# Kernel tuning notes

Measured on AMD Instinct MI355X. Metric: run time of the kernel, lower is better.

Reference implementation:

```python
import jax, jax.numpy as jnp
import numpy as np

N_EMBD = 384
NUM_HEADS = 6
HEAD_SIZE = 64


def setup_inputs() -> dict:
    key = jax.random.key(0)
    k1, k2, k3, k4 = jax.random.split(key, 4)
    B, T = 32, 1024
    x = jax.random.normal(k1, (B, T, N_EMBD), dtype=jnp.float32)
    # torch Linear(n_embd, 3*n_embd, bias=False): store as [in, out]
    s_attn = 1.0 / np.sqrt(N_EMBD)
    W_attn = jax.random.uniform(k2, (N_EMBD, 3 * N_EMBD), dtype=jnp.float32, minval=-s_attn, maxval=s_attn)
    W_proj = jax.random.uniform(k3, (N_EMBD, N_EMBD), dtype=jnp.float32, minval=-s_attn, maxval=s_attn)
    b_proj = jax.random.uniform(k4, (N_EMBD,), dtype=jnp.float32, minval=-s_attn, maxval=s_attn)
    return {"x": x, "W_attn": W_attn, "W_proj": W_proj, "b_proj": b_proj}


def reference(x, W_attn, W_proj, b_proj):
    B, T, C = x.shape
    H, D = NUM_HEADS, HEAD_SIZE
    qkv = x @ W_attn                      # [B, T, 3C]
    q, k, v = jnp.split(qkv, 3, axis=2)   # each [B, T, C]
    # [B, H, T, D]
    q = q.reshape(B, T, H, D).transpose(0, 2, 1, 3)
    k = k.reshape(B, T, H, D).transpose(0, 2, 1, 3)
    v = v.reshape(B, T, H, D).transpose(0, 2, 1, 3)
    scale = 1.0 / jnp.sqrt(jnp.asarray(D, dtype=x.dtype))
    scores = jnp.einsum("bhqd,bhkd->bhqk", q, k) * scale  # [B, H, T, T]
    causal = jnp.tril(jnp.ones((T, T), dtype=bool))
    scores = jnp.where(causal, scores, jnp.asarray(-jnp.inf, dtype=scores.dtype))
    attn = jax.nn.softmax(scores, axis=-1)
    y = jnp.einsum("bhqk,bhkd->bhqd", attn, v)             # [B, H, T, D]
    y = y.transpose(0, 2, 1, 3).reshape(B, T, C)
    # dropout is inactive in eval mode
    return y @ W_proj + b_proj
```

## Files before the change

### kernel.cpp

```cpp
#include <hip/hip_runtime.h>
#include <hip/hip_bf16.h>

#define DEV __device__ __forceinline__

typedef __attribute__((ext_vector_type(4))) float f32x4;
typedef __bf16 bf16x8 __attribute__((ext_vector_type(8)));

static DEV unsigned short f2bf(float f) {
    union { float f; unsigned u; } x; x.f = f;
    unsigned r = x.u + 0x7fffu + ((x.u >> 16) & 1u);
    return (unsigned short)(r >> 16);
}

static DEV f32x4 zero4() { f32x4 v; v[0] = 0.f; v[1] = 0.f; v[2] = 0.f; v[3] = 0.f; return v; }

#define GL1(p) ((const __attribute__((address_space(1))) void*)(p))
#define LDS3(p) ((__attribute__((address_space(3))) void*)(p))


__global__ __launch_bounds__(256) void k_prep(
    const float* __restrict__ x, unsigned short* __restrict__ xb,
    const float* __restrict__ Wa, unsigned short* __restrict__ WaT,
    const float* __restrict__ Wp, unsigned short* __restrict__ WpT)
{
    int i = blockIdx.x * 256 + threadIdx.x;
    if (i < 3145728) {
        float4 v = reinterpret_cast<const float4*>(x)[i];
        ushort4 o;
        o.x = f2bf(v.x); o.y = f2bf(v.y); o.z = f2bf(v.z); o.w = f2bf(v.w);
        reinterpret_cast<ushort4*>(xb)[i] = o;
    } else if (i < 3145728 + 442368) {
        int j = i - 3145728;
        int n = j / 384, k = j - n * 384;
        WaT[j] = f2bf(Wa[(size_t)k * 1152 + n]);
    } else if (i < 3145728 + 442368 + 147456) {
        int j = i - (3145728 + 442368);
        int n = j / 384, k = j - n * 384;
        WpT[j] = f2bf(Wp[(size_t)k * 384 + n]);
    }
}


template <int SWAP>
static DEV void gemm_mainloop(
    const unsigned short* __restrict__ A,
    const unsigned short* __restrict__ B,
    int m0, int n0, int tid,
    f32x4 (&acc)[4][4],
    unsigned short (&lA)[128][64], unsigned short (&lB)[128][64])
{
    const int K = 384;
    const int w = tid >> 6, lane = tid & 63;
    const int wm = (w >> 1) * 64, wn = (w & 1) * 64;
    const int lr = lane & 15, lg = lane >> 4;
    const int lrow = lane >> 3;
    const int lcol = ((lane & 7) ^ lrow) * 8;

    for (int kb = 0; kb < K; kb += 64) {
        __syncthreads();
#pragma unroll
        for (int c = 0; c < 4; ++c) {
            int rb = (w * 4 + c) * 8;
            __builtin_amdgcn_global_load_lds(GL1(&A[(size_t)(m0 + rb + lrow) * K + kb + lcol]),
                                             LDS3(&lA[rb][0]), 16, 0, 0);
            __builtin_amdgcn_global_load_lds(GL1(&B[(size_t)(n0 + rb + lrow) * K + kb + lcol]),
                                             LDS3(&lB[rb][0]), 16, 0, 0);
        }
        __syncthreads();

        bf16x8 af[4][2], bfr[4][2];
#pragma unroll
        for (int kc = 0; kc < 2; ++kc) {
#pragma unroll
            for (int t = 0; t < 4; ++t) {
                int ga = ((kc * 4 + lg) ^ (lr & 7)) * 8;
                af[t][kc]  = *(const bf16x8*)&lA[wm + t * 16 + lr][ga];
                bfr[t][kc] = *(const bf16x8*)&lB[wn + t * 16 + lr][ga];
            }
        }
#pragma unroll
        for (int kc = 0; kc < 2; ++kc)
#pragma unroll
            for (int mt = 0; mt < 4; ++mt)
#pragma unroll
                for (int nt = 0; nt < 4; ++nt)
                    acc[mt][nt] = SWAP
                        ? __builtin_amdgcn_mfma_f32_16x16x32_bf16(bfr[nt][kc], af[mt][kc], acc[mt][nt], 0, 0, 0)
                        : __builtin_amdgcn_mfma_f32_16x16x32_bf16(af[mt][kc], bfr[nt][kc], acc[mt][nt], 0, 0, 0);
    }
}


__global__ __launch_bounds__(256) void k_gemm_qkv(
    const unsigned short* __restrict__ A,
    const unsigned short* __restrict__ B,
    unsigned short* __restrict__ Qb, unsigned short* __restrict__ Kb,
    unsigned short* __restrict__ Vb)
{
    __shared__ unsigned short lA[128][64];
    __shared__ unsigned short lB[128][64];

    const int tid = threadIdx.x;
    const int m0 = blockIdx.x * 128, n0 = blockIdx.y * 128;
    const int w = tid >> 6, lane = tid & 63;
    const int wm = (w >> 1) * 64, wn = (w & 1) * 64;
    const int lr = lane & 15, lg = lane >> 4;

    f32x4 acc[4][4];
#pragma unroll
    for (int i = 0; i < 4; i++)
#pragma unroll
        for (int j = 0; j < 4; j++) acc[i][j] = zero4();

    if (blockIdx.y < 6) {
        gemm_mainloop<1>(A, B, m0, n0, tid, acc, lA, lB);
        const int which = blockIdx.y / 3;
#pragma unroll
        for (int mt = 0; mt < 4; ++mt) {
            int row = m0 + wm + mt * 16 + lr;
            int bb = row >> 10, tloc = row & 1023;
#pragma unroll
            for (int nt = 0; nt < 4; ++nt) {
                int col = n0 + wn + nt * 16 + lg * 4;
                int c = col - which * 384;
                int hh = c >> 6, d0 = c & 63;
                size_t bh = (size_t)bb * 6 + hh;
                int kc = (d0 >> 5) & 1;
                int ln = (tloc & 15) + 16 * ((d0 >> 3) & 3);
                int e0 = d0 & 7;
                union { __bf16 h4[4]; uint2 u; } pk;
                if (which == 0) {
#pragma unroll
                    for (int r = 0; r < 4; ++r)
                        pk.h4[r] = (__bf16)(acc[mt][nt][r] * 0.18033688f);
                    int qt = tloc >> 5, fmt = (tloc >> 4) & 1;
                    *(uint2*)&Qb[((((bh * 32 + qt) * 2 + fmt) * 2 + kc) * 64 + ln) * 8 + e0] = pk.u;
                } else {
#pragma unroll
                    for (int r = 0; r < 4; ++r)
                        pk.h4[r] = (__bf16)acc[mt][nt][r];
                    int ktt = tloc >> 6, fnt = (tloc >> 4) & 3;
                    *(uint2*)&Kb[((((bh * 16 + ktt) * 4 + fnt) * 2 + kc) * 64 + ln) * 8 + e0] = pk.u;
                }
            }
        }
    } else {
        gemm_mainloop<0>(A, B, m0, n0, tid, acc, lA, lB);
#pragma unroll
        for (int nt = 0; nt < 4; ++nt) {
            int col = n0 + wn + nt * 16 + lr;
            int c = col - 768;
            int hh = c >> 6, d = c & 63;
            int fnt = d >> 4;
#pragma unroll
            for (int mt = 0; mt < 4; ++mt) {
                int row0 = m0 + wm + mt * 16 + lg * 4;
                int bb = row0 >> 10, t0 = row0 & 1023;
                size_t bh = (size_t)bb * 6 + hh;
                int ktt = t0 >> 6, kc = (t0 >> 5) & 1, e0 = t0 & 7;
                int ln = (d & 15) + 16 * ((t0 >> 3) & 3);
                union { __bf16 h4[4]; uint2 u; } pk;
#pragma unroll
                for (int r = 0; r < 4; ++r)
                    pk.h4[r] = (__bf16)acc[mt][nt][r];
                *(uint2*)&Vb[((((bh * 16 + ktt) * 4 + fnt) * 2 + kc) * 64 + ln) * 8 + e0] = pk.u;
            }
        }
    }
}


__global__ __launch_bounds__(256) void k_gemm_proj(
    const unsigned short* __restrict__ A,
    const unsigned short* __restrict__ B,
    const float* __restrict__ bias, float* __restrict__ Out)
{
    __shared__ unsigned short lA[128][64];
    __shared__ unsigned short lB[128][64];

    const int tid = threadIdx.x;
    const int m0 = blockIdx.x * 128, n0 = blockIdx.y * 128;
    const int w = tid >> 6, lane = tid & 63;
    const int wm = (w >> 1) * 64, wn = (w & 1) * 64;
    const int lr = lane & 15, lg = lane >> 4;

    f32x4 acc[4][4];
#pragma unroll
    for (int i = 0; i < 4; i++)
#pragma unroll
        for (int j = 0; j < 4; j++) acc[i][j] = zero4();

    gemm_mainloop<1>(A, B, m0, n0, tid, acc, lA, lB);

#pragma unroll
    for (int mt = 0; mt < 4; ++mt) {
        int row = m0 + wm + mt * 16 + lr;
#pragma unroll
        for (int nt = 0; nt < 4; ++nt) {
            int col = n0 + wn + nt * 16 + lg * 4;
            f32x4 bv = *(const f32x4*)&bias[col];
            f32x4 ov;
#pragma unroll
            for (int r = 0; r < 4; ++r) ov[r] = acc[mt][nt][r] + bv[r];
            *(f32x4*)&Out[(size_t)row * 384 + col] = ov;
        }
    }
}


template <int NTM, bool MASK>
static DEV void attn_tile(
    const unsigned short* lKt, const unsigned short* lVt, unsigned short* lPw,
    const bf16x8 (&qf)[2][2], f32x4 (&o)[2][4], float (&ls)[2],
    int kt, int qw, int lane)
{
    constexpr int KCM = NTM / 2;
    const int lr = lane & 15, lg = lane >> 4;

    bf16x8 kf[NTM][2];
#pragma unroll
    for (int nt = 0; nt < NTM; ++nt)
#pragma unroll
        for (int kc = 0; kc < 2; ++kc)
            kf[nt][kc] = *(const bf16x8*)&lKt[(nt * 2 + kc) * 512 + lane * 8];

    bf16x8 vf[4][KCM];
#pragma unroll
    for (int nt = 0; nt < 4; ++nt)
#pragma unroll
        for (int kc = 0; kc < KCM; ++kc)
            vf[nt][kc] = *(const bf16x8*)&lVt[(nt * 2 + kc) * 512 + lane * 8];

    f32x4 st[2][NTM];
#pragma unroll
    for (int mt = 0; mt < 2; ++mt)
#pragma unroll
        for (int nt = 0; nt < NTM; ++nt) st[mt][nt] = zero4();

#pragma unroll
    for (int kc = 0; kc < 2; ++kc)
#pragma unroll
        for (int mt = 0; mt < 2; ++mt)
#pragma unroll
            for (int nt = 0; nt < NTM; ++nt)
                st[mt][nt] = __builtin_amdgcn_mfma_f32_16x16x32_bf16(kf[nt][kc], qf[mt][kc], st[mt][nt], 0, 0, 0);

#pragma unroll
    for (int mt = 0; mt < 2; ++mt) {
#pragma unroll
        for (int nt = 0; nt < NTM; ++nt) {
            union { __bf16 hh[4]; uint2 u; } pk;
            float e[4];
#pragma unroll
            for (int r = 0; r < 4; ++r) {
                float ev = __builtin_amdgcn_exp2f(st[mt][nt][r]);
                if (MASK) {
                    int kg = kt * 64 + nt * 16 + lg * 4 + r;
                    int qg = qw + mt * 16 + lr;
                    if (kg > qg) ev = 0.f;
                }
                e[r] = ev;
                pk.hh[r] = (__bf16)ev;
            }
            ls[mt] += (e[0] + e[1]) + (e[2] + e[3]);
            int ln2 = lr + 16 * ((nt & 1) * 2 + (lg >> 1));
            *(uint2*)&lPw[(mt * 2 + (nt >> 1)) * 512 + ln2 * 8 + (lg & 1) * 4] = pk.u;
        }
    }

    bf16x8 pf[2][KCM];
#pragma unroll
    for (int mt = 0; mt < 2; ++mt)
#pragma unroll
        for (int kc = 0; kc < KCM; ++kc)
            pf[mt][kc] = *(const bf16x8*)&lPw[(mt * 2 + kc) * 512 + lane * 8];

#pragma unroll
    for (int mt = 0; mt < 2; ++mt)
#pragma unroll
        for (int nt = 0; nt < 4; ++nt)
#pragma unroll
            for (int kc = 0; kc < KCM; ++kc)
                o[mt][nt] = __builtin_amdgcn_mfma_f32_16x16x32_bf16(pf[mt][kc], vf[nt][kc], o[mt][nt], 0, 0, 0);
}

__global__ __launch_bounds__(256, 3) void k_attn(
    const unsigned short* __restrict__ Qf,
    const unsigned short* __restrict__ Kf,
    const unsigned short* __restrict__ Vf,
    unsigned short* __restrict__ Y)
{
    __shared__ unsigned short lK[2][4096];
    __shared__ unsigned short lV[2][4096];
    __shared__ unsigned short lPf[4][2048];

    const int tid = threadIdx.x;
    const int w = tid >> 6, lane = tid & 63;
    const int lr = lane & 15, lg = lane >> 4;
    const int bh = blockIdx.x;
    const int g = 7 - blockIdx.y;
    const int qt = 4 * g + w;
    const int qw = qt * 32;
    const int nkt = qt / 2 + 1;
    const int nsteps = 2 * g + 2;
    const int b = bh / 6, h = bh - b * 6;

    const unsigned short* Kbh = Kf + (size_t)bh * 65536;
    const unsigned short* Vbh = Vf + (size_t)bh * 65536;

    bf16x8 qf[2][2];
#pragma unroll
    for (int mt = 0; mt < 2; ++mt)
#pragma unroll
        for (int kc = 0; kc < 2; ++kc)
            qf[mt][kc] = *(const bf16x8*)&Qf[((((size_t)bh * 32 + qt) * 2 + mt) * 2 + kc) * 512 + lane * 8];

    f32x4 o[2][4];
    float ls[2] = {0.f, 0.f};
#pragma unroll
    for (int mt = 0; mt < 2; ++mt)
#pragma unroll
        for (int nt = 0; nt < 4; ++nt) o[mt][nt] = zero4();

#pragma unroll
    for (int i = 0; i < 2; ++i) {
        __builtin_amdgcn_global_load_lds(GL1(Kbh + (size_t)w * 1024 + i * 512 + lane * 8),
                                         LDS3(&lK[0][w * 1024 + i * 512]), 16, 0, 0);
        __builtin_amdgcn_global_load_lds(GL1(Vbh + (size_t)w * 1024 + i * 512 + lane * 8),
                                         LDS3(&lV[0][w * 1024 + i * 512]), 16, 0, 0);
    }

    for (int kt = 0; kt < nsteps; ++kt) {
        __syncthreads();
        if (kt + 1 < nsteps) {
            int nb = (kt + 1) & 1;
#pragma unroll
            for (int i = 0; i < 2; ++i) {
                __builtin_amdgcn_global_load_lds(GL1(Kbh + (size_t)(kt + 1) * 4096 + w * 1024 + i * 512 + lane * 8),
                                                 LDS3(&lK[nb][w * 1024 + i * 512]), 16, 0, 0);
                __builtin_amdgcn_global_load_lds(GL1(Vbh + (size_t)(kt + 1) * 4096 + w * 1024 + i * 512 + lane * 8),
                                                 LDS3(&lV[nb][w * 1024 + i * 512]), 16, 0, 0);
            }
        }
        if (kt < nkt) {
            const unsigned short* lKt = lK[kt & 1];
            const unsigned short* lVt = lV[kt & 1];
            if (kt == nkt - 1) {
                if (qt & 1) attn_tile<4, true>(lKt, lVt, lPf[w], qf, o, ls, kt, qw, lane);
                else        attn_tile<2, true>(lKt, lVt, lPf[w], qf, o, ls, kt, qw, lane);
            } else {
                attn_tile<4, false>(lKt, lVt, lPf[w], qf, o, ls, kt, qw, lane);
            }
        }
    }

    float inv[2];
#pragma unroll
    for (int mt = 0; mt < 2; ++mt) {
        float s = ls[mt];
        s += __shfl_xor(s, 16);
        s += __shfl_xor(s, 32);
        inv[mt] = 1.0f / s;
    }
#pragma unroll
    for (int mt = 0; mt < 2; ++mt) {
        float iv[4];
#pragma unroll
        for (int r = 0; r < 4; ++r) iv[r] = __shfl(inv[mt], lg * 4 + r);
#pragma unroll
        for (int nt = 0; nt < 4; ++nt)
#pragma unroll
            for (int r = 0; r < 4; ++r) {
                int qrow = qw + mt * 16 + lg * 4 + r;
                int col = h * 64 + nt * 16 + lr;
                Y[((size_t)b * 1024 + qrow) * 384 + col] = f2bf(o[mt][nt][r] * iv[r]);
            }
    }
}


extern "C" void kernel_launch(void* const* d_in, const int* in_sizes, int n_in,
                              void* d_out, int out_size, void* d_ws, size_t ws_size,
                              hipStream_t stream)
{
    const float* x  = (const float*)d_in[0];
    const float* Wa = (const float*)d_in[1];
    const float* Wp = (const float*)d_in[2];
    const float* bp = (const float*)d_in[3];
    float* out = (float*)d_out;

    char* ws = (char*)d_ws;
    unsigned short* xb  = (unsigned short*)(ws);
    unsigned short* WaT = (unsigned short*)(ws + 25165824);
    unsigned short* WpT = (unsigned short*)(ws + 26050560);
    unsigned short* Qb  = (unsigned short*)(ws + 26345472);
    unsigned short* Kb  = (unsigned short*)(ws + 51511296);
    unsigned short* Vtb = (unsigned short*)(ws + 76677120);

    k_prep<<<14592, 256, 0, stream>>>(x, xb, Wa, WaT, Wp, WpT);
    k_gemm_qkv<<<dim3(256, 9), 256, 0, stream>>>(xb, WaT, Qb, Kb, Vtb);
    k_attn<<<dim3(192, 8), 256, 0, stream>>>(Qb, Kb, Vtb, xb);
    k_gemm_proj<<<dim3(256, 3), 256, 0, stream>>>(xb, WpT, bp, out);
}
```

Before: 125.1 us.

## Double-buffer GEMM LDS loads, raise MFMA priority, and transpose attention output accumulation

The GEMM mainloop gets double-buffered LDS tiles, so the next K slice is loaded while the current one is computed, and one barrier per iteration is removed. The attention PV MFMA swaps its operands, so the output accumulator is laid out with the query row on lr. That lets the epilogue write four contiguous bf16 values per store and drops the per-element shuffles. s_setprio is raised around the MFMA blocks to favour issuing matrix instructions. Doubling the GEMM LDS use may lower occupancy, and the single barrier per iteration relies on the async LDS loads finishing before the next sync.

```diff
diff --git a/kernel.cpp b/kernel.cpp
--- a/kernel.cpp
+++ b/kernel.cpp
@@ -47,7 +47,7 @@
     const unsigned short* __restrict__ B,
     int m0, int n0, int tid,
     f32x4 (&acc)[4][4],
-    unsigned short (&lA)[128][64], unsigned short (&lB)[128][64])
+    unsigned short (&lA)[2][128][64], unsigned short (&lB)[2][128][64])
 {
     const int K = 384;
     const int w = tid >> 6, lane = tid & 63;
@@ -56,17 +56,24 @@
     const int lrow = lane >> 3;
     const int lcol = ((lane & 7) ^ lrow) * 8;
 
-    for (int kb = 0; kb < K; kb += 64) {
+#define STAGE_GEMM(buf, kb)                                                                       \
+    {                                                                                             \
+        _Pragma("unroll") for (int c = 0; c < 4; ++c) {                                           \
+            int rb = (w * 4 + c) * 8;                                                             \
+            __builtin_amdgcn_global_load_lds(GL1(&A[(size_t)(m0 + rb + lrow) * K + (kb) + lcol]), \
+                                             LDS3(&lA[buf][rb][0]), 16, 0, 0);                    \
+            __builtin_amdgcn_global_load_lds(GL1(&B[(size_t)(n0 + rb + lrow) * K + (kb) + lcol]), \
+                                             LDS3(&lB[buf][rb][0]), 16, 0, 0);                    \
+        }                                                                                         \
+    }
+
+    STAGE_GEMM(0, 0);
+
+#pragma unroll
+    for (int ks = 0; ks < 6; ++ks) {
         __syncthreads();
-#pragma unroll
-        for (int c = 0; c < 4; ++c) {
-            int rb = (w * 4 + c) * 8;
-            __builtin_amdgcn_global_load_lds(GL1(&A[(size_t)(m0 + rb + lrow) * K + kb + lcol]),
-                                             LDS3(&lA[rb][0]), 16, 0, 0);
-            __builtin_amdgcn_global_load_lds(GL1(&B[(size_t)(n0 + rb + lrow) * K + kb + lcol]),
-                                             LDS3(&lB[rb][0]), 16, 0, 0);
-        }
-        __syncthreads();
+        if (ks < 5) STAGE_GEMM((ks + 1) & 1, (ks + 1) * 64);
+        const int cur = ks & 1;
 
         bf16x8 af[4][2], bfr[4][2];
 #pragma unroll
@@ -74,8 +81,8 @@
 #pragma unroll
             for (int t = 0; t < 4; ++t) {
                 int ga = ((kc * 4 + lg) ^ (lr & 7)) * 8;
-                af[t][kc]  = *(const bf16x8*)&lA[wm + t * 16 + lr][ga];
-                bfr[t][kc] = *(const bf16x8*)&lB[wn + t * 16 + lr][ga];
+                af[t][kc]  = *(const bf16x8*)&lA[cur][wm + t * 16 + lr][ga];
+                bfr[t][kc] = *(const bf16x8*)&lB[cur][wn + t * 16 + lr][ga];
             }
         }
 #pragma unroll
@@ -88,6 +95,7 @@
                         ? __builtin_amdgcn_mfma_f32_16x16x32_bf16(bfr[nt][kc], af[mt][kc], acc[mt][nt], 0, 0, 0)
                         : __builtin_amdgcn_mfma_f32_16x16x32_bf16(af[mt][kc], bfr[nt][kc], acc[mt][nt], 0, 0, 0);
     }
+#undef STAGE_GEMM
 }
 
 
@@ -97,8 +105,8 @@
     unsigned short* __restrict__ Qb, unsigned short* __restrict__ Kb,
     unsigned short* __restrict__ Vb)
 {
-    __shared__ unsigned short lA[128][64];
-    __shared__ unsigned short lB[128][64];
+    __shared__ unsigned short lA[2][128][64];
+    __shared__ unsigned short lB[2][128][64];
 
     const int tid = threadIdx.x;
     const int m0 = blockIdx.x * 128, n0 = blockIdx.y * 128;
@@ -175,8 +183,8 @@
     const unsigned short* __restrict__ B,
     const float* __restrict__ bias, float* __restrict__ Out)
 {
-    __shared__ unsigned short lA[128][64];
-    __shared__ unsigned short lB[128][64];
+    __shared__ unsigned short lA[2][128][64];
+    __shared__ unsigned short lB[2][128][64];
 
     const int tid = threadIdx.x;
     const int m0 = blockIdx.x * 128, n0 = blockIdx.y * 128;
@@ -237,6 +245,7 @@
 #pragma unroll
         for (int nt = 0; nt < NTM; ++nt) st[mt][nt] = zero4();
 
+    __builtin_amdgcn_s_setprio(1);
 #pragma unroll
     for (int kc = 0; kc < 2; ++kc)
 #pragma unroll
@@ -244,6 +253,7 @@
 #pragma unroll
             for (int nt = 0; nt < NTM; ++nt)
                 st[mt][nt] = __builtin_amdgcn_mfma_f32_16x16x32_bf16(kf[nt][kc], qf[mt][kc], st[mt][nt], 0, 0, 0);
+    __builtin_amdgcn_s_setprio(0);
 
 #pragma unroll
     for (int mt = 0; mt < 2; ++mt) {
@@ -275,13 +285,15 @@
         for (int kc = 0; kc < KCM; ++kc)
             pf[mt][kc] = *(const bf16x8*)&lPw[(mt * 2 + kc) * 512 + lane * 8];
 
+    __builtin_amdgcn_s_setprio(1);
 #pragma unroll
     for (int mt = 0; mt < 2; ++mt)
 #pragma unroll
         for (int nt = 0; nt < 4; ++nt)
 #pragma unroll
             for (int kc = 0; kc < KCM; ++kc)
-                o[mt][nt] = __builtin_amdgcn_mfma_f32_16x16x32_bf16(pf[mt][kc], vf[nt][kc], o[mt][nt], 0, 0, 0);
+                o[mt][nt] = __builtin_amdgcn_mfma_f32_16x16x32_bf16(vf[nt][kc], pf[mt][kc], o[mt][nt], 0, 0, 0);
+    __builtin_amdgcn_s_setprio(0);
 }
 
 __global__ __launch_bounds__(256, 3) void k_attn(
@@ -364,17 +376,13 @@
     }
 #pragma unroll
     for (int mt = 0; mt < 2; ++mt) {
-        float iv[4];
-#pragma unroll
-        for (int r = 0; r < 4; ++r) iv[r] = __shfl(inv[mt], lg * 4 + r);
-#pragma unroll
-        for (int nt = 0; nt < 4; ++nt)
-#pragma unroll
-            for (int r = 0; r < 4; ++r) {
-                int qrow = qw + mt * 16 + lg * 4 + r;
-                int col = h * 64 + nt * 16 + lr;
-                Y[((size_t)b * 1024 + qrow) * 384 + col] = f2bf(o[mt][nt][r] * iv[r]);
-            }
+#pragma unroll
+        for (int nt = 0; nt < 4; ++nt) {
+            union { __bf16 h4[4]; uint2 u; } pk;
+#pragma unroll
+            for (int r = 0; r < 4; ++r) pk.h4[r] = (__bf16)(o[mt][nt][r] * inv[mt]);
+            *(uint2*)&Y[((size_t)b * 1024 + qw + mt * 16 + lr) * 384 + h * 64 + nt * 16 + lg * 4] = pk.u;
+        }
     }
 }
 
```

After: 131.7 us. 1.05x slower.

## Pair causal query groups per block and swap MFMA operands for vector stores

Applied to the files above, without the earlier changes.

Each attention block now handles two complementary query-tile groups (g and 7-g) one after the other. Every block therefore does a similar amount of causal work, and the grid shrinks from 8 to 4 groups per head. The PV MFMA operands are swapped so the output accumulator is transposed, which lets each lane pack four bf16 results into one 8-byte store instead of doing scalar stores with shuffles. s_setprio is raised around the MFMA bursts to favour matrix issue; the cost is fewer blocks to fill the GPU and an extra sync between the two passes.

```diff
diff --git a/kernel.cpp b/kernel.cpp
--- a/kernel.cpp
+++ b/kernel.cpp
@@ -237,6 +237,7 @@
 #pragma unroll
         for (int nt = 0; nt < NTM; ++nt) st[mt][nt] = zero4();
 
+    __builtin_amdgcn_s_setprio(1);
 #pragma unroll
     for (int kc = 0; kc < 2; ++kc)
 #pragma unroll
@@ -244,6 +245,7 @@
 #pragma unroll
             for (int nt = 0; nt < NTM; ++nt)
                 st[mt][nt] = __builtin_amdgcn_mfma_f32_16x16x32_bf16(kf[nt][kc], qf[mt][kc], st[mt][nt], 0, 0, 0);
+    __builtin_amdgcn_s_setprio(0);
 
 #pragma unroll
     for (int mt = 0; mt < 2; ++mt) {
@@ -275,13 +277,98 @@
         for (int kc = 0; kc < KCM; ++kc)
             pf[mt][kc] = *(const bf16x8*)&lPw[(mt * 2 + kc) * 512 + lane * 8];
 
+    __builtin_amdgcn_s_setprio(1);
 #pragma unroll
     for (int mt = 0; mt < 2; ++mt)
 #pragma unroll
         for (int nt = 0; nt < 4; ++nt)
 #pragma unroll
             for (int kc = 0; kc < KCM; ++kc)
-                o[mt][nt] = __builtin_amdgcn_mfma_f32_16x16x32_bf16(pf[mt][kc], vf[nt][kc], o[mt][nt], 0, 0, 0);
+                o[mt][nt] = __builtin_amdgcn_mfma_f32_16x16x32_bf16(vf[nt][kc], pf[mt][kc], o[mt][nt], 0, 0, 0);
+    __builtin_amdgcn_s_setprio(0);
+}
+
+static DEV void attn_pass(
+    int gg, int w, int lane, int b, int h, int bh,
+    const unsigned short* __restrict__ Qf,
+    const unsigned short* __restrict__ Kbh,
+    const unsigned short* __restrict__ Vbh,
+    unsigned short* __restrict__ Y,
+    unsigned short (&lK)[2][4096], unsigned short (&lV)[2][4096],
+    unsigned short* lPw)
+{
+    const int lr = lane & 15, lg = lane >> 4;
+    const int qt = 4 * gg + w;
+    const int qw = qt * 32;
+    const int nkt = qt / 2 + 1;
+    const int nsteps = 2 * gg + 2;
+
+    bf16x8 qf[2][2];
+#pragma unroll
+    for (int mt = 0; mt < 2; ++mt)
+#pragma unroll
+        for (int kc = 0; kc < 2; ++kc)
+            qf[mt][kc] = *(const bf16x8*)&Qf[((((size_t)bh * 32 + qt) * 2 + mt) * 2 + kc) * 512 + lane * 8];
+
+    f32x4 o[2][4];
+    float ls[2] = {0.f, 0.f};
+#pragma unroll
+    for (int mt = 0; mt < 2; ++mt)
+#pragma unroll
+        for (int nt = 0; nt < 4; ++nt) o[mt][nt] = zero4();
+
+    __syncthreads();
+
+#pragma unroll
+    for (int i = 0; i < 2; ++i) {
+        __builtin_amdgcn_global_load_lds(GL1(Kbh + (size_t)w * 1024 + i * 512 + lane * 8),
+                                         LDS3(&lK[0][w * 1024 + i * 512]), 16, 0, 0);
+        __builtin_amdgcn_global_load_lds(GL1(Vbh + (size_t)w * 1024 + i * 512 + lane * 8),
+                                         LDS3(&lV[0][w * 1024 + i * 512]), 16, 0, 0);
+    }
+
+    for (int kt = 0; kt < nsteps; ++kt) {
+        __syncthreads();
+        if (kt + 1 < nsteps) {
+            int nb = (kt + 1) & 1;
+#pragma unroll
+            for (int i = 0; i < 2; ++i) {
+                __builtin_amdgcn_global_load_lds(GL1(Kbh + (size_t)(kt + 1) * 4096 + w * 1024 + i * 512 + lane * 8),
+                                                 LDS3(&lK[nb][w * 1024 + i * 512]), 16, 0, 0);
+                __builtin_amdgcn_global_load_lds(GL1(Vbh + (size_t)(kt + 1) * 4096 + w * 1024 + i * 512 + lane * 8),
+                                                 LDS3(&lV[nb][w * 1024 + i * 512]), 16, 0, 0);
+            }
+        }
+        if (kt < nkt) {
+            const unsigned short* lKt = lK[kt & 1];
+            const unsigned short* lVt = lV[kt & 1];
+            if (kt == nkt - 1) {
+                if (qt & 1) attn_tile<4, true>(lKt, lVt, lPw, qf, o, ls, kt, qw, lane);
+                else        attn_tile<2, true>(lKt, lVt, lPw, qf, o, ls, kt, qw, lane);
+            } else {
+                attn_tile<4, false>(lKt, lVt, lPw, qf, o, ls, kt, qw, lane);
+            }
+        }
+    }
+
+    float inv[2];
+#pragma unroll
+    for (int mt = 0; mt < 2; ++mt) {
+        float s = ls[mt];
+        s += __shfl_xor(s, 16);
+        s += __shfl_xor(s, 32);
+        inv[mt] = 1.0f / s;
+    }
+#pragma unroll
+    for (int mt = 0; mt < 2; ++mt) {
+#pragma unroll
+        for (int nt = 0; nt < 4; ++nt) {
+            union { __bf16 h4[4]; uint2 u; } pk;
+#pragma unroll
+            for (int r = 0; r < 4; ++r) pk.h4[r] = (__bf16)(o[mt][nt][r] * inv[mt]);
+            *(uint2*)&Y[((size_t)b * 1024 + qw + mt * 16 + lr) * 384 + h * 64 + nt * 16 + lg * 4] = pk.u;
+        }
+    }
 }
 
 __global__ __launch_bounds__(256, 3) void k_attn(
@@ -296,86 +383,15 @@
 
     const int tid = threadIdx.x;
     const int w = tid >> 6, lane = tid & 63;
-    const int lr = lane & 15, lg = lane >> 4;
     const int bh = blockIdx.x;
-    const int g = 7 - blockIdx.y;
-    const int qt = 4 * g + w;
-    const int qw = qt * 32;
-    const int nkt = qt / 2 + 1;
-    const int nsteps = 2 * g + 2;
+    const int g = blockIdx.y;
     const int b = bh / 6, h = bh - b * 6;
 
     const unsigned short* Kbh = Kf + (size_t)bh * 65536;
     const unsigned short* Vbh = Vf + (size_t)bh * 65536;
 
-    bf16x8 qf[2][2];
-#pragma unroll
-    for (int mt = 0; mt < 2; ++mt)
-#pragma unroll
-        for (int kc = 0; kc < 2; ++kc)
-            qf[mt][kc] = *(const bf16x8*)&Qf[((((size_t)bh * 32 + qt) * 2 + mt) * 2 + kc) * 512 + lane * 8];
-
-    f32x4 o[2][4];
-    float ls[2] = {0.f, 0.f};
-#pragma unroll
-    for (int mt = 0; mt < 2; ++mt)
-#pragma unroll
-        for (int nt = 0; nt < 4; ++nt) o[mt][nt] = zero4();
-
-#pragma unroll
-    for (int i = 0; i < 2; ++i) {
-        __builtin_amdgcn_global_load_lds(GL1(Kbh + (size_t)w * 1024 + i * 512 + lane * 8),
-                                         LDS3(&lK[0][w * 1024 + i * 512]), 16, 0, 0);
-        __builtin_amdgcn_global_load_lds(GL1(Vbh + (size_t)w * 1024 + i * 512 + lane * 8),
-                                         LDS3(&lV[0][w * 1024 + i * 512]), 16, 0, 0);
-    }
-
-    for (int kt = 0; kt < nsteps; ++kt) {
-        __syncthreads();
-        if (kt + 1 < nsteps) {
-            int nb = (kt + 1) & 1;
-#pragma unroll
-            for (int i = 0; i < 2; ++i) {
-                __builtin_amdgcn_global_load_lds(GL1(Kbh + (size_t)(kt + 1) * 4096 + w * 1024 + i * 512 + lane * 8),
-                                                 LDS3(&lK[nb][w * 1024 + i * 512]), 16, 0, 0);
-                __builtin_amdgcn_global_load_lds(GL1(Vbh + (size_t)(kt + 1) * 4096 + w * 1024 + i * 512 + lane * 8),
-                                                 LDS3(&lV[nb][w * 1024 + i * 512]), 16, 0, 0);
-            }
-        }
-        if (kt < nkt) {
-            const unsigned short* lKt = lK[kt & 1];
-            const unsigned short* lVt = lV[kt & 1];
-            if (kt == nkt - 1) {
-                if (qt & 1) attn_tile<4, true>(lKt, lVt, lPf[w], qf, o, ls, kt, qw, lane);
-                else        attn_tile<2, true>(lKt, lVt, lPf[w], qf, o, ls, kt, qw, lane);
-            } else {
-                attn_tile<4, false>(lKt, lVt, lPf[w], qf, o, ls, kt, qw, lane);
-            }
-        }
-    }
-
-    float inv[2];
-#pragma unroll
-    for (int mt = 0; mt < 2; ++mt) {
-        float s = ls[mt];
-        s += __shfl_xor(s, 16);
-        s += __shfl_xor(s, 32);
-        inv[mt] = 1.0f / s;
-    }
-#pragma unroll
-    for (int mt = 0; mt < 2; ++mt) {
-        float iv[4];
-#pragma unroll
-        for (int r = 0; r < 4; ++r) iv[r] = __shfl(inv[mt], lg * 4 + r);
-#pragma unroll
-        for (int nt = 0; nt < 4; ++nt)
-#pragma unroll
-            for (int r = 0; r < 4; ++r) {
-                int qrow = qw + mt * 16 + lg * 4 + r;
-                int col = h * 64 + nt * 16 + lr;
-                Y[((size_t)b * 1024 + qrow) * 384 + col] = f2bf(o[mt][nt][r] * iv[r]);
-            }
-    }
+    attn_pass(g,     w, lane, b, h, bh, Qf, Kbh, Vbh, Y, lK, lV, lPf[w]);
+    attn_pass(7 - g, w, lane, b, h, bh, Qf, Kbh, Vbh, Y, lK, lV, lPf[w]);
 }
 
 
@@ -399,6 +415,6 @@
 
     k_prep<<<14592, 256, 0, stream>>>(x, xb, Wa, WaT, Wp, WpT);
     k_gemm_qkv<<<dim3(256, 9), 256, 0, stream>>>(xb, WaT, Qb, Kb, Vtb);
-    k_attn<<<dim3(192, 8), 256, 0, stream>>>(Qb, Kb, Vtb, xb);
+    k_attn<<<dim3(192, 4), 256, 0, stream>>>(Qb, Kb, Vtb, xb);
     k_gemm_proj<<<dim3(256, 3), 256, 0, stream>>>(xb, WpT, bp, out);
 }
```

Result: no change. 124.8 us (-0.2%).
